# Kernel tuning notes

Measured on AMD Instinct MI355X. Metric: run time of the kernel, lower is better.

Reference implementation:

```python
import jax, jax.numpy as jnp
import numpy as np

B, T, S = 4, 2048, 512
HID, ND, NH = 2048, 1024, 16
HD = HID // NH  # 128
GATING_INIT = -4.0


def setup_inputs() -> dict:
    key = jax.random.key(0)
    ks = jax.random.split(key, 12)
    sc_h = 1.0 / np.sqrt(HID)
    sc_n = 1.0 / np.sqrt(ND)
    mask = jax.random.bernoulli(ks[2], 0.9, (B, S))
    mask = mask.at[:, 0].set(True)  # avoid fully-masked rows (NaN softmax)
    return {
        "hidden_states": jax.random.normal(ks[0], (B, T, HID), jnp.float32),
        "notes": jax.random.normal(ks[1], (B, S, ND), jnp.float32),
        "notes_mask": mask,
        "q_w": jax.random.normal(ks[3], (HID, HID), jnp.float32) * sc_h,
        "q_b": jax.random.normal(ks[4], (HID,), jnp.float32) * 0.01,
        "k_w": jax.random.normal(ks[5], (HID, ND), jnp.float32) * sc_n,
        "k_b": jax.random.normal(ks[6], (HID,), jnp.float32) * 0.01,
        "v_w": jax.random.normal(ks[7], (HID, ND), jnp.float32) * sc_n,
        "v_b": jax.random.normal(ks[8], (HID,), jnp.float32) * 0.01,
        "o_w": jax.random.normal(ks[9], (HID, HID), jnp.float32) * sc_h,
        "o_b": jax.random.normal(ks[10], (HID,), jnp.float32) * 0.01,
        "gate": jnp.full((1,), GATING_INIT, jnp.float32),
    }


def reference(hidden_states, notes, notes_mask, q_w, q_b, k_w, k_b, v_w, v_b, o_w, o_b, gate):
    # projections (torch Linear: x @ W^T + b)
    q = hidden_states @ q_w.T + q_b            # (B,T,HID)
    k = notes @ k_w.T + k_b                    # (B,S,HID)
    v = notes @ v_w.T + v_b                    # (B,S,HID)
    q = q.reshape(B, T, NH, HD).transpose(0, 2, 1, 3)  # (B,H,T,D)
    k = k.reshape(B, S, NH, HD).transpose(0, 2, 1, 3)  # (B,H,S,D)
    v = v.reshape(B, S, NH, HD).transpose(0, 2, 1, 3)
    scores = jnp.einsum("bhtd,bhsd->bhts", q, k) / jnp.sqrt(jnp.float32(HD))
    scores = jnp.where(notes_mask[:, None, None, :], scores, -jnp.inf)
    attn = jax.nn.softmax(scores, axis=-1)
    context = jnp.einsum("bhts,bhsd->bhtd", attn, v)   # (B,H,T,D)
    g = jax.nn.sigmoid(gate).reshape(1, 1, 1, 1)
    context = (g * context).transpose(0, 2, 1, 3).reshape(B, T, HID)
    delta = context @ o_w.T + o_b
    return delta
```

## Files before the change

kernel.cpp:

```cpp
#include <hip/hip_runtime.h>
#include <hip/hip_bf16.h>
#include <stdint.h>

#define B_ 4
#define T_ 2048
#define S_ 512
#define HID_ 2048
#define ND_ 1024
#define NH_ 16
#define HD_ 128

typedef unsigned short u16;
typedef __attribute__((ext_vector_type(8))) short bf16x8;
typedef __attribute__((ext_vector_type(4))) float f32x4;
typedef __attribute__((ext_vector_type(4))) float f4;
typedef __attribute__((ext_vector_type(4))) u16 us4;
typedef __attribute__((ext_vector_type(8))) u16 us8;

__device__ inline u16 f2bf(float f) {
  unsigned u = __builtin_bit_cast(unsigned, f);
  u += 0x7FFFu + ((u >> 16) & 1u);
  return (u16)(u >> 16);
}

__device__ inline f32x4 mfma16(bf16x8 a, bf16x8 b, f32x4 c) {
  return __builtin_amdgcn_mfma_f32_16x16x32_bf16(a, b, c, 0, 0, 0);
}

__device__ inline void gload_lds16(const u16* g, u16* l) {
  __builtin_amdgcn_global_load_lds(
      (const __attribute__((address_space(1))) unsigned int*)g,
      (__attribute__((address_space(3))) unsigned int*)l, 16, 0, 0);
}

__global__ __launch_bounds__(256) void convert_all(
    const float* __restrict__ h, const float* __restrict__ n,
    const float* __restrict__ qw, const float* __restrict__ kw,
    const float* __restrict__ vw, const float* __restrict__ ow,
    u16* __restrict__ dh, u16* __restrict__ dn, u16* __restrict__ dqw,
    u16* __restrict__ dkw, u16* __restrict__ dvw, u16* __restrict__ dow) {
  const int C0 = 4194304;
  const int C1 = C0 + 524288;
  const int C2 = C1 + 1048576;
  const int C3 = C2 + 524288;
  const int C4 = C3 + 524288;
  const int C5 = C4 + 1048576;
  for (int c = blockIdx.x * blockDim.x + threadIdx.x; c < C5;
       c += gridDim.x * blockDim.x) {
    const float* s; u16* d; int o;
    if (c < C0)      { s = h;  d = dh;  o = c; }
    else if (c < C1) { s = n;  d = dn;  o = c - C0; }
    else if (c < C2) { s = qw; d = dqw; o = c - C1; }
    else if (c < C3) { s = kw; d = dkw; o = c - C2; }
    else if (c < C4) { s = vw; d = dvw; o = c - C3; }
    else             { s = ow; d = dow; o = c - C4; }
    f4 v = ((const f4*)s)[o];
    us4 r = { f2bf(v[0]), f2bf(v[1]), f2bf(v[2]), f2bf(v[3]) };
    ((us4*)d)[o] = r;
  }
}

template <bool OUT_BF16>
__global__ __launch_bounds__(256) void gemm_bt(
    const u16* __restrict__ A, const u16* __restrict__ Bm,
    const float* __restrict__ bias, void* __restrict__ Cout,
    int M, int N, int K) {
  __shared__ u16 As[128 * 32];
  __shared__ u16 Bs[128 * 32];
  const int tid = threadIdx.x;
  const int lane = tid & 63;
  const int wave = tid >> 6;
  const int wr = (wave >> 1) * 64;
  const int wc = (wave & 1) * 64;
  const int c15 = lane & 15;
  const int g = lane >> 4;
  const int bx = blockIdx.x, by = blockIdx.y;

  const u16* gA = A + (size_t)(by * 128 + (tid >> 2)) * K + (tid & 3) * 8;
  const u16* gB = Bm + (size_t)(bx * 128 + (tid >> 2)) * K + (tid & 3) * 8;

  f32x4 acc[4][4];
#pragma unroll
  for (int i = 0; i < 4; ++i)
#pragma unroll
    for (int j = 0; j < 4; ++j) acc[i][j] = (f32x4){0.f, 0.f, 0.f, 0.f};

  for (int k0 = 0; k0 < K; k0 += 32) {
    gload_lds16(gA + k0, &As[wave * 512]);
    gload_lds16(gA + (size_t)64 * K + k0, &As[2048 + wave * 512]);
    gload_lds16(gB + k0, &Bs[wave * 512]);
    gload_lds16(gB + (size_t)64 * K + k0, &Bs[2048 + wave * 512]);
    __syncthreads();
    bf16x8 af[4], bfr[4];
#pragma unroll
    for (int mt = 0; mt < 4; ++mt)
      af[mt] = *(const bf16x8*)&As[(wr + mt * 16 + c15) * 32 + g * 8];
#pragma unroll
    for (int nt = 0; nt < 4; ++nt)
      bfr[nt] = *(const bf16x8*)&Bs[(wc + nt * 16 + c15) * 32 + g * 8];
#pragma unroll
    for (int mt = 0; mt < 4; ++mt)
#pragma unroll
      for (int nt = 0; nt < 4; ++nt)
        acc[mt][nt] = mfma16(af[mt], bfr[nt], acc[mt][nt]);
    __syncthreads();
  }

#pragma unroll
  for (int mt = 0; mt < 4; ++mt)
#pragma unroll
    for (int nt = 0; nt < 4; ++nt) {
      const int m = by * 128 + wr + mt * 16 + g * 4;
      const int n = bx * 128 + wc + nt * 16 + c15;
      const float bv = bias[n];
#pragma unroll
      for (int r = 0; r < 4; ++r) {
        const float v = acc[mt][nt][r] + bv;
        if (OUT_BF16)
          ((u16*)Cout)[(size_t)(m + r) * N + n] = f2bf(v);
        else
          ((float*)Cout)[(size_t)(m + r) * N + n] = v;
      }
    }
}

template <bool OUT_BF16>
__global__ __launch_bounds__(512, 2) void gemm256(
    const u16* __restrict__ A, const u16* __restrict__ Bm,
    const float* __restrict__ bias, void* __restrict__ Cout,
    int M, int N, int K) {
  extern __shared__ u16 lds[];
  const int tid = threadIdx.x;
  const int lane = tid & 63, wave = tid >> 6;
  const int wm = wave >> 2, wn = wave & 3;
  const int c15 = lane & 15, g = lane >> 4;
  const int bn = blockIdx.x, bm = blockIdx.y;
  const int NT = K >> 5;

  const int srow = tid >> 2;
  const int sx = (tid & 3) ^ ((srow >> 1) & 3);
  const u16* pa0 = A + (size_t)(bm * 256 + srow) * K + sx * 8;
  const u16* pa1 = A + (size_t)(bm * 256 + 128 + srow) * K + sx * 8;
  const u16* pb0 = Bm + (size_t)(bn * 256 + srow) * K + sx * 8;
  const u16* pb1 = Bm + (size_t)(bn * 256 + 128 + srow) * K + sx * 8;

  const int xr = (c15 >> 1) & 3;
  const int aoff = wm * 4096 + c15 * 32 + ((g ^ xr)) * 8;
  const int boff = 8192 + wn * 2048 + c15 * 32 + ((g ^ xr)) * 8;

  f32x4 acc[8][4];
#pragma unroll
  for (int i = 0; i < 8; ++i)
#pragma unroll
    for (int j = 0; j < 4; ++j) acc[i][j] = (f32x4){0.f, 0.f, 0.f, 0.f};

  {
    u16* sA = lds + wave * 512;
    u16* sB = lds + 8192 + wave * 512;
    gload_lds16(pa0, sA);          gload_lds16(pa1, sA + 4096);
    gload_lds16(pb0, sB);          gload_lds16(pb1, sB + 4096);
    pa0 += 32; pa1 += 32; pb0 += 32; pb1 += 32;
    gload_lds16(pa0, sA + 16384);  gload_lds16(pa1, sA + 20480);
    gload_lds16(pb0, sB + 16384);  gload_lds16(pb1, sB + 20480);
    pa0 += 32; pa1 += 32; pb0 += 32; pb1 += 32;
  }
  asm volatile("s_waitcnt vmcnt(4)" ::: "memory");
  __builtin_amdgcn_s_barrier();
  __builtin_amdgcn_sched_barrier(0);

  int curo = 0, stgo = 32768;
  for (int t = 0; t < NT; ++t) {
    const bool more = (t + 2 < NT);
    const u16* cb = lds + curo;
    bf16x8 a[4], b[4];
#pragma unroll
    for (int mf = 0; mf < 4; ++mf)
      a[mf] = *(const bf16x8*)(cb + aoff + mf * 512);
#pragma unroll
    for (int nf = 0; nf < 4; ++nf)
      b[nf] = *(const bf16x8*)(cb + boff + nf * 512);
    if (more) {
      gload_lds16(pa0, lds + stgo + wave * 512);
      gload_lds16(pa1, lds + stgo + 4096 + wave * 512);
    }
    __builtin_amdgcn_s_barrier();
    __builtin_amdgcn_sched_barrier(0);
    __builtin_amdgcn_s_setprio(1);
#pragma unroll
    for (int mf = 0; mf < 4; ++mf)
#pragma unroll
      for (int nf = 0; nf < 4; ++nf)
        acc[mf][nf] = mfma16(a[mf], b[nf], acc[mf][nf]);
    __builtin_amdgcn_s_setprio(0);
    __builtin_amdgcn_s_barrier();
    __builtin_amdgcn_sched_barrier(0);
    bf16x8 a2[4];
#pragma unroll
    for (int mf = 0; mf < 4; ++mf)
      a2[mf] = *(const bf16x8*)(cb + aoff + (4 + mf) * 512);
    if (more) {
      gload_lds16(pb0, lds + stgo + 8192 + wave * 512);
      gload_lds16(pb1, lds + stgo + 12288 + wave * 512);
      pa0 += 32; pa1 += 32; pb0 += 32; pb1 += 32;
    }
    __builtin_amdgcn_s_barrier();
    __builtin_amdgcn_sched_barrier(0);
    __builtin_amdgcn_s_setprio(1);
#pragma unroll
    for (int mf = 0; mf < 4; ++mf)
#pragma unroll
      for (int nf = 0; nf < 4; ++nf)
        acc[4 + mf][nf] = mfma16(a2[mf], b[nf], acc[4 + mf][nf]);
    __builtin_amdgcn_s_setprio(0);
    if (t < NT - 1) {
      if (more) asm volatile("s_waitcnt vmcnt(4)" ::: "memory");
      else      asm volatile("s_waitcnt vmcnt(0)" ::: "memory");
    }
    __builtin_amdgcn_s_barrier();
    __builtin_amdgcn_sched_barrier(0);
    curo = (curo == 32768) ? 0 : curo + 16384;
    stgo = (stgo == 32768) ? 0 : stgo + 16384;
  }

#pragma unroll
  for (int mf = 0; mf < 8; ++mf)
#pragma unroll
    for (int nf = 0; nf < 4; ++nf) {
      const int m = bm * 256 + wm * 128 + mf * 16 + g * 4;
      const int n = bn * 256 + wn * 64 + nf * 16 + c15;
      const float bv = bias[n];
#pragma unroll
      for (int r = 0; r < 4; ++r) {
        const float v = acc[mf][nf][r] + bv;
        if (OUT_BF16)
          ((u16*)Cout)[(size_t)(m + r) * N + n] = f2bf(v);
        else
          ((float*)Cout)[(size_t)(m + r) * N + n] = v;
      }
    }
}

__global__ __launch_bounds__(256) void transpose_v(const u16* __restrict__ v,
                                                   u16* __restrict__ vt) {
  __shared__ u16 tile[32][36];
  const int s0 = blockIdx.x * 32;
  const int bh = blockIdx.y;
  const int d0 = blockIdx.z * 32;
  const int b = bh >> 4, h = bh & 15;
  const int tid = threadIdx.x;
  const int sl = tid >> 3, dl = (tid & 7) * 4;
  us4 val = *(const us4*)(v + (size_t)(b * S_ + s0 + sl) * HID_ + h * HD_ + d0 + dl);
  *(us4*)&tile[sl][dl] = val;
  __syncthreads();
  const int dl2 = tid >> 3, sl2 = (tid & 7) * 4;
  us4 outv = { tile[sl2 + 0][dl2], tile[sl2 + 1][dl2],
               tile[sl2 + 2][dl2], tile[sl2 + 3][dl2] };
  *(us4*)(vt + ((size_t)bh * HD_ + d0 + dl2) * S_ + s0 + sl2) = outv;
}

__global__ __launch_bounds__(256) void attn_fwd(
    const u16* __restrict__ q, const u16* __restrict__ k,
    const u16* __restrict__ vt, const int* __restrict__ mask,
    const float* __restrict__ gate, u16* __restrict__ ctx) {
  __shared__ u16 smem[16384];
  __shared__ float addend[S_];
  __shared__ u16 p_lds[4][16][40];
  const int tid = threadIdx.x, lane = tid & 63, wave = tid >> 6;
  const int bh = blockIdx.y, b = bh >> 4, h = bh & 15;
  const int t0 = blockIdx.x * 64 + wave * 16;
  const int c15 = lane & 15, g = lane >> 4;

  const u16* kb  = k + (size_t)b * S_ * HID_ + h * HD_;
  const u16* vtb = vt + (size_t)bh * HD_ * S_;

  const u16* sp[4];
  int dj[4];
  u16* ldsbase;
  ptrdiff_t stride;
  if (wave < 2) {
    ldsbase = smem;
    stride = 32 * HID_;
#pragma unroll
    for (int i = 0; i < 4; ++i) {
      const int jj = wave * 4 + i;
      const int row = jj * 4 + (lane >> 4);
      const int cb = (lane & 15) * 16;
      const int cbp = cb ^ ((row & 7) << 4);
      sp[i] = kb + (size_t)row * HID_ + (cbp >> 1);
      dj[i] = jj * 512;
    }
  } else {
    ldsbase = smem + 8192;
    stride = 32;
#pragma unroll
    for (int i = 0; i < 4; ++i) {
      const int jj = (wave - 2) * 4 + i;
      const int row = jj * 8 + (lane >> 3);
      const int cb = (lane & 7) * 16;
      const int cbp = cb ^ ((row & 7) << 4);
      const int d = row * 2 + (cbp >> 6);
      sp[i] = vtb + (size_t)d * S_ + ((cbp & 63) >> 1);
      dj[i] = jj * 512;
    }
  }
#define STAGE(cur)                                            \
  do {                                                        \
    _Pragma("unroll") for (int i_ = 0; i_ < 4; ++i_) {        \
      gload_lds16(sp[i_], ldsbase + (cur) * 4096 + dj[i_]);   \
      sp[i_] += stride;                                       \
    }                                                         \
  } while (0)

  STAGE(0);

  for (int s = tid; s < S_; s += 256)
    addend[s] = mask[b * S_ + s] ? 0.f : -1e30f;

  const u16* qrow = q + (size_t)(b * T_ + t0 + c15) * HID_ + h * HD_;
  bf16x8 qf[4];
#pragma unroll
  for (int dc = 0; dc < 4; ++dc)
    qf[dc] = *(const bf16x8*)&qrow[dc * 32 + g * 8];

  const int ksw = (c15 & 7) << 4;
  int kcol[4];
#pragma unroll
  for (int dc = 0; dc < 4; ++dc)
    kcol[dc] = ((dc * 64 + g * 16) ^ ksw) >> 1;
  const int krow0 = c15 * 128, krow1 = (16 + c15) * 128;
  const int vsw = ((c15 >> 1) & 7) << 4;
  const int vcol = (((c15 & 1) * 64 + g * 16) ^ vsw) >> 1;
  const int vrow = (c15 >> 1) * 64;

  float m_run = -1e30f, l_run = 0.f;
  f32x4 ct[8];
#pragma unroll
  for (int i = 0; i < 8; ++i) ct[i] = (f32x4){0.f, 0.f, 0.f, 0.f};
  const float scale = 0.08838834764831845f;

  __syncthreads();

  for (int it = 0; it < 16; ++it) {
    const int cur = it & 1;
    if (it < 15) STAGE(cur ^ 1);
    const int s0 = it * 32;
    const u16* kt = smem + cur * 4096;
    const u16* vl = smem + 8192 + cur * 4096;

    f32x4 st0 = {0.f, 0.f, 0.f, 0.f}, st1 = {0.f, 0.f, 0.f, 0.f};
    __builtin_amdgcn_s_setprio(1);
#pragma unroll
    for (int dc = 0; dc < 4; ++dc) {
      bf16x8 ka0 = *(const bf16x8*)&kt[krow0 + kcol[dc]];
      bf16x8 ka1 = *(const bf16x8*)&kt[krow1 + kcol[dc]];
      st0 = mfma16(ka0, qf[dc], st0);
      st1 = mfma16(ka1, qf[dc], st1);
    }
    __builtin_amdgcn_s_setprio(0);

    float sc[8];
#pragma unroll
    for (int r = 0; r < 4; ++r) {
      sc[r]     = st0[r] * scale + addend[s0 + g * 4 + r];
      sc[4 + r] = st1[r] * scale + addend[s0 + 16 + g * 4 + r];
    }
    float tm = sc[0];
#pragma unroll
    for (int i = 1; i < 8; ++i) tm = fmaxf(tm, sc[i]);
    tm = fmaxf(tm, __shfl_xor(tm, 16));
    tm = fmaxf(tm, __shfl_xor(tm, 32));
    const float nm = fmaxf(m_run, tm);
    if (!__all(nm - m_run <= 8.f)) {
      const float corr = __expf(m_run - nm);
      l_run *= corr;
#pragma unroll
      for (int dt = 0; dt < 8; ++dt)
#pragma unroll
        for (int r = 0; r < 4; ++r) ct[dt][r] *= corr;
      m_run = nm;
    }
    float p[8], ps = 0.f;
#pragma unroll
    for (int i = 0; i < 8; ++i) { p[i] = __expf(sc[i] - m_run); ps += p[i]; }
    ps += __shfl_xor(ps, 16);
    ps += __shfl_xor(ps, 32);
    l_run += ps;

    us4 pk0 = { f2bf(p[0]), f2bf(p[1]), f2bf(p[2]), f2bf(p[3]) };
    us4 pk1 = { f2bf(p[4]), f2bf(p[5]), f2bf(p[6]), f2bf(p[7]) };
    *(us4*)&p_lds[wave][c15][g * 4] = pk0;
    *(us4*)&p_lds[wave][c15][16 + g * 4] = pk1;
    bf16x8 pf = *(const bf16x8*)&p_lds[wave][c15][g * 8];

    __builtin_amdgcn_s_setprio(1);
#pragma unroll
    for (int dt = 0; dt < 8; ++dt) {
      bf16x8 vf = *(const bf16x8*)&vl[(dt * 8) * 64 + vrow + vcol];
      ct[dt] = mfma16(vf, pf, ct[dt]);
    }
    __builtin_amdgcn_s_setprio(0);

    __syncthreads();
  }
#undef STAGE

  const float gsig = 1.f / (1.f + __expf(-gate[0]));
  const float inv = gsig / l_run;
  u16* c_lds = smem + wave * (16 * 136);
#pragma unroll
  for (int dt = 0; dt < 8; ++dt) {
    us4 o = { f2bf(ct[dt][0] * inv), f2bf(ct[dt][1] * inv),
              f2bf(ct[dt][2] * inv), f2bf(ct[dt][3] * inv) };
    *(us4*)&c_lds[c15 * 136 + dt * 16 + g * 4] = o;
  }
  u16* crow = ctx + (size_t)(b * T_ + t0) * HID_ + h * HD_;
#pragma unroll
  for (int rep = 0; rep < 4; ++rep) {
    const int tt = g + rep * 4;
    us8 valv = *(const us8*)&c_lds[tt * 136 + c15 * 8];
    *(us8*)&crow[(size_t)tt * HID_ + c15 * 8] = valv;
  }
}

extern "C" void kernel_launch(void* const* d_in, const int* in_sizes, int n_in,
                              void* d_out, int out_size, void* d_ws, size_t ws_size,
                              hipStream_t stream) {
  (void)in_sizes; (void)n_in; (void)out_size; (void)ws_size;
  const float* hs   = (const float*)d_in[0];
  const float* nts  = (const float*)d_in[1];
  const int*   mask = (const int*)d_in[2];
  const float* qw   = (const float*)d_in[3];
  const float* qb   = (const float*)d_in[4];
  const float* kw   = (const float*)d_in[5];
  const float* kbi  = (const float*)d_in[6];
  const float* vw   = (const float*)d_in[7];
  const float* vbi  = (const float*)d_in[8];
  const float* ow   = (const float*)d_in[9];
  const float* obi  = (const float*)d_in[10];
  const float* gate = (const float*)d_in[11];
  float* out = (float*)d_out;

  char* w = (char*)d_ws;
  u16* h_bf   = (u16*)(w + 0);
  u16* n_bf   = (u16*)(w + 33554432);
  u16* qw_bf  = (u16*)(w + 37748736);
  u16* kw_bf  = (u16*)(w + 46137344);
  u16* vw_bf  = (u16*)(w + 50331648);
  u16* ow_bf  = (u16*)(w + 54525952);
  u16* q_bf   = (u16*)(w + 62914560);
  u16* k_bf   = (u16*)(w + 96468992);
  u16* v_bf   = (u16*)(w + 104857600);
  u16* vt_bf  = (u16*)(w + 113246208);
  u16* ctx_bf = h_bf;

  hipFuncSetAttribute(reinterpret_cast<const void*>(&gemm256<true>),
                      hipFuncAttributeMaxDynamicSharedMemorySize, 98304);
  hipFuncSetAttribute(reinterpret_cast<const void*>(&gemm256<false>),
                      hipFuncAttributeMaxDynamicSharedMemorySize, 98304);

  convert_all<<<dim3(2048), dim3(256), 0, stream>>>(
      hs, nts, qw, kw, vw, ow, h_bf, n_bf, qw_bf, kw_bf, vw_bf, ow_bf);
  gemm_bt<true><<<dim3(16, 16), dim3(256), 0, stream>>>(
      n_bf, kw_bf, kbi, k_bf, 2048, 2048, 1024);
  gemm_bt<true><<<dim3(16, 16), dim3(256), 0, stream>>>(
      n_bf, vw_bf, vbi, v_bf, 2048, 2048, 1024);
  transpose_v<<<dim3(16, 64, 4), dim3(256), 0, stream>>>(v_bf, vt_bf);
  gemm256<true><<<dim3(8, 32), dim3(512), 98304, stream>>>(
      h_bf, qw_bf, qb, q_bf, 8192, 2048, 2048);
  attn_fwd<<<dim3(32, 64), dim3(256), 0, stream>>>(
      q_bf, k_bf, vt_bf, mask, gate, ctx_bf);
  gemm256<false><<<dim3(8, 32), dim3(512), 98304, stream>>>(
      ctx_bf, ow_bf, obi, out, 8192, 2048, 2048);
}
```

Measured before the change: 303.1 us.

## Switch attention to 32x32 MFMA with register P exchange; swizzle GEMM block order

The attention kernel now gives each wave 32 query rows and uses 32x32x16 bf16 MFMA for both QK^T and PV. The shared-memory round trip for P is replaced by packed bf16 conversion and a cross-half lane shuffle, and the V tile layout and swizzle are reworked to match. This halves the attention grid and cuts LDS traffic and reduction shuffles, at the cost of more registers per wave. The 256-tile GEMM also remaps block indices so consecutive blocks share B-matrix columns, aiming for better L2 reuse.

```diff
diff --git a/kernel.cpp b/kernel.cpp
--- a/kernel.cpp
+++ b/kernel.cpp
@@ -11,11 +11,14 @@
 #define HD_ 128
 
 typedef unsigned short u16;
+typedef unsigned int u32;
 typedef __attribute__((ext_vector_type(8))) short bf16x8;
 typedef __attribute__((ext_vector_type(4))) float f32x4;
+typedef __attribute__((ext_vector_type(16))) float f32x16;
 typedef __attribute__((ext_vector_type(4))) float f4;
 typedef __attribute__((ext_vector_type(4))) u16 us4;
 typedef __attribute__((ext_vector_type(8))) u16 us8;
+typedef __attribute__((ext_vector_type(4))) u32 u32x4;
 
 __device__ inline u16 f2bf(float f) {
   unsigned u = __builtin_bit_cast(unsigned, f);
@@ -23,8 +26,17 @@
   return (u16)(u >> 16);
 }
 
+__device__ inline u32 cvtpk(float lo, float hi) {
+  u32 r;
+  asm("v_cvt_pk_bf16_f32 %0, %1, %2" : "=v"(r) : "v"(lo), "v"(hi));
+  return r;
+}
+
 __device__ inline f32x4 mfma16(bf16x8 a, bf16x8 b, f32x4 c) {
   return __builtin_amdgcn_mfma_f32_16x16x32_bf16(a, b, c, 0, 0, 0);
+}
+__device__ inline f32x16 mfma32(bf16x8 a, bf16x8 b, f32x16 c) {
+  return __builtin_amdgcn_mfma_f32_32x32x16_bf16(a, b, c, 0, 0, 0);
 }
 
 __device__ inline void gload_lds16(const u16* g, u16* l) {
@@ -134,7 +146,9 @@
   const int lane = tid & 63, wave = tid >> 6;
   const int wm = wave >> 2, wn = wave & 3;
   const int c15 = lane & 15, g = lane >> 4;
-  const int bn = blockIdx.x, bm = blockIdx.y;
+  const int bid = blockIdx.y * gridDim.x + blockIdx.x;
+  const int sw = (bid & 7) * 32 + (bid >> 3);
+  const int bn = sw & 7, bm = sw >> 3;
   const int NT = K >> 5;
 
   const int srow = tid >> 2;
@@ -262,13 +276,12 @@
     const u16* __restrict__ q, const u16* __restrict__ k,
     const u16* __restrict__ vt, const int* __restrict__ mask,
     const float* __restrict__ gate, u16* __restrict__ ctx) {
-  __shared__ u16 smem[16384];
+  __shared__ u16 smem[17408];
   __shared__ float addend[S_];
-  __shared__ u16 p_lds[4][16][40];
   const int tid = threadIdx.x, lane = tid & 63, wave = tid >> 6;
   const int bh = blockIdx.y, b = bh >> 4, h = bh & 15;
-  const int t0 = blockIdx.x * 64 + wave * 16;
-  const int c15 = lane & 15, g = lane >> 4;
+  const int tw = blockIdx.x * 128 + wave * 32;
+  const int l31 = lane & 31, hi = lane >> 5;
 
   const u16* kb  = k + (size_t)b * S_ * HID_ + h * HD_;
   const u16* vtb = vt + (size_t)bh * HD_ * S_;
@@ -295,11 +308,10 @@
 #pragma unroll
     for (int i = 0; i < 4; ++i) {
       const int jj = (wave - 2) * 4 + i;
-      const int row = jj * 8 + (lane >> 3);
-      const int cb = (lane & 7) * 16;
-      const int cbp = cb ^ ((row & 7) << 4);
-      const int d = row * 2 + (cbp >> 6);
-      sp[i] = vtb + (size_t)d * S_ + ((cbp & 63) >> 1);
+      const int d = jj * 16 + (lane >> 2);
+      const int cb = (lane & 3) * 16;
+      const int cbp = cb ^ ((d & 3) << 4);
+      sp[i] = vtb + (size_t)d * S_ + (cbp >> 1);
       dj[i] = jj * 512;
     }
   }
@@ -316,26 +328,25 @@
   for (int s = tid; s < S_; s += 256)
     addend[s] = mask[b * S_ + s] ? 0.f : -1e30f;
 
-  const u16* qrow = q + (size_t)(b * T_ + t0 + c15) * HID_ + h * HD_;
-  bf16x8 qf[4];
-#pragma unroll
-  for (int dc = 0; dc < 4; ++dc)
-    qf[dc] = *(const bf16x8*)&qrow[dc * 32 + g * 8];
-
-  const int ksw = (c15 & 7) << 4;
-  int kcol[4];
-#pragma unroll
-  for (int dc = 0; dc < 4; ++dc)
-    kcol[dc] = ((dc * 64 + g * 16) ^ ksw) >> 1;
-  const int krow0 = c15 * 128, krow1 = (16 + c15) * 128;
-  const int vsw = ((c15 >> 1) & 7) << 4;
-  const int vcol = (((c15 & 1) * 64 + g * 16) ^ vsw) >> 1;
-  const int vrow = (c15 >> 1) * 64;
+  const u16* qrow = q + (size_t)(b * T_ + tw + l31) * HID_ + h * HD_;
+  bf16x8 qf[8];
+#pragma unroll
+  for (int dc = 0; dc < 8; ++dc)
+    qf[dc] = *(const bf16x8*)&qrow[dc * 16 + hi * 8];
+
+  int kofs[8];
+#pragma unroll
+  for (int dc = 0; dc < 8; ++dc)
+    kofs[dc] = l31 * 128 + (((dc * 32 + hi * 16) ^ ((l31 & 7) << 4)) >> 1);
+  const int vcol0 = ((hi * 16) ^ ((l31 & 3) << 4)) >> 1;
+  const int vcol1 = ((32 + hi * 16) ^ ((l31 & 3) << 4)) >> 1;
 
   float m_run = -1e30f, l_run = 0.f;
-  f32x4 ct[8];
-#pragma unroll
-  for (int i = 0; i < 8; ++i) ct[i] = (f32x4){0.f, 0.f, 0.f, 0.f};
+  f32x16 ct[4];
+#pragma unroll
+  for (int i = 0; i < 4; ++i)
+#pragma unroll
+    for (int r = 0; r < 16; ++r) ct[i][r] = 0.f;
   const float scale = 0.08838834764831845f;
 
   __syncthreads();
@@ -347,56 +358,67 @@
     const u16* kt = smem + cur * 4096;
     const u16* vl = smem + 8192 + cur * 4096;
 
-    f32x4 st0 = {0.f, 0.f, 0.f, 0.f}, st1 = {0.f, 0.f, 0.f, 0.f};
+    f32x16 st;
+#pragma unroll
+    for (int r = 0; r < 16; ++r) st[r] = 0.f;
     __builtin_amdgcn_s_setprio(1);
 #pragma unroll
-    for (int dc = 0; dc < 4; ++dc) {
-      bf16x8 ka0 = *(const bf16x8*)&kt[krow0 + kcol[dc]];
-      bf16x8 ka1 = *(const bf16x8*)&kt[krow1 + kcol[dc]];
-      st0 = mfma16(ka0, qf[dc], st0);
-      st1 = mfma16(ka1, qf[dc], st1);
+    for (int dc = 0; dc < 8; ++dc) {
+      bf16x8 kf = *(const bf16x8*)&kt[kofs[dc]];
+      st = mfma32(kf, qf[dc], st);
     }
     __builtin_amdgcn_s_setprio(0);
 
-    float sc[8];
-#pragma unroll
-    for (int r = 0; r < 4; ++r) {
-      sc[r]     = st0[r] * scale + addend[s0 + g * 4 + r];
-      sc[4 + r] = st1[r] * scale + addend[s0 + 16 + g * 4 + r];
+    float sc[16];
+#pragma unroll
+    for (int rq = 0; rq < 4; ++rq) {
+      f4 ad = *(const f4*)&addend[s0 + rq * 8 + hi * 4];
+#pragma unroll
+      for (int m = 0; m < 4; ++m)
+        sc[rq * 4 + m] = st[rq * 4 + m] * scale + ad[m];
     }
     float tm = sc[0];
 #pragma unroll
-    for (int i = 1; i < 8; ++i) tm = fmaxf(tm, sc[i]);
-    tm = fmaxf(tm, __shfl_xor(tm, 16));
+    for (int i = 1; i < 16; ++i) tm = fmaxf(tm, sc[i]);
     tm = fmaxf(tm, __shfl_xor(tm, 32));
     const float nm = fmaxf(m_run, tm);
     if (!__all(nm - m_run <= 8.f)) {
       const float corr = __expf(m_run - nm);
       l_run *= corr;
 #pragma unroll
-      for (int dt = 0; dt < 8; ++dt)
-#pragma unroll
-        for (int r = 0; r < 4; ++r) ct[dt][r] *= corr;
+      for (int db = 0; db < 4; ++db)
+#pragma unroll
+        for (int r = 0; r < 16; ++r) ct[db][r] *= corr;
       m_run = nm;
     }
-    float p[8], ps = 0.f;
-#pragma unroll
-    for (int i = 0; i < 8; ++i) { p[i] = __expf(sc[i] - m_run); ps += p[i]; }
-    ps += __shfl_xor(ps, 16);
+    float p[16], ps = 0.f;
+#pragma unroll
+    for (int i = 0; i < 16; ++i) { p[i] = __expf(sc[i] - m_run); ps += p[i]; }
     ps += __shfl_xor(ps, 32);
     l_run += ps;
 
-    us4 pk0 = { f2bf(p[0]), f2bf(p[1]), f2bf(p[2]), f2bf(p[3]) };
-    us4 pk1 = { f2bf(p[4]), f2bf(p[5]), f2bf(p[6]), f2bf(p[7]) };
-    *(us4*)&p_lds[wave][c15][g * 4] = pk0;
-    *(us4*)&p_lds[wave][c15][16 + g * 4] = pk1;
-    bf16x8 pf = *(const bf16x8*)&p_lds[wave][c15][g * 8];
+    u32 w[8], x[8];
+#pragma unroll
+    for (int q2 = 0; q2 < 4; ++q2) {
+      w[2 * q2]     = cvtpk(p[4 * q2],     p[4 * q2 + 1]);
+      w[2 * q2 + 1] = cvtpk(p[4 * q2 + 2], p[4 * q2 + 3]);
+    }
+#pragma unroll
+    for (int i = 0; i < 8; ++i) x[i] = __shfl_xor((int)w[i], 32);
+    const u32x4 f0 = hi ? (u32x4){x[2], x[3], w[2], w[3]}
+                        : (u32x4){w[0], w[1], x[0], x[1]};
+    const u32x4 f1 = hi ? (u32x4){x[6], x[7], w[6], w[7]}
+                        : (u32x4){w[4], w[5], x[4], x[5]};
+    const bf16x8 pf0 = __builtin_bit_cast(bf16x8, f0);
+    const bf16x8 pf1 = __builtin_bit_cast(bf16x8, f1);
 
     __builtin_amdgcn_s_setprio(1);
 #pragma unroll
-    for (int dt = 0; dt < 8; ++dt) {
-      bf16x8 vf = *(const bf16x8*)&vl[(dt * 8) * 64 + vrow + vcol];
-      ct[dt] = mfma16(vf, pf, ct[dt]);
+    for (int db = 0; db < 4; ++db) {
+      bf16x8 vf0 = *(const bf16x8*)&vl[db * 1024 + l31 * 32 + vcol0];
+      ct[db] = mfma32(vf0, pf0, ct[db]);
+      bf16x8 vf1 = *(const bf16x8*)&vl[db * 1024 + l31 * 32 + vcol1];
+      ct[db] = mfma32(vf1, pf1, ct[db]);
     }
     __builtin_amdgcn_s_setprio(0);
 
@@ -406,19 +428,21 @@
 
   const float gsig = 1.f / (1.f + __expf(-gate[0]));
   const float inv = gsig / l_run;
-  u16* c_lds = smem + wave * (16 * 136);
-#pragma unroll
-  for (int dt = 0; dt < 8; ++dt) {
-    us4 o = { f2bf(ct[dt][0] * inv), f2bf(ct[dt][1] * inv),
-              f2bf(ct[dt][2] * inv), f2bf(ct[dt][3] * inv) };
-    *(us4*)&c_lds[c15 * 136 + dt * 16 + g * 4] = o;
-  }
-  u16* crow = ctx + (size_t)(b * T_ + t0) * HID_ + h * HD_;
-#pragma unroll
-  for (int rep = 0; rep < 4; ++rep) {
-    const int tt = g + rep * 4;
-    us8 valv = *(const us8*)&c_lds[tt * 136 + c15 * 8];
-    *(us8*)&crow[(size_t)tt * HID_ + c15 * 8] = valv;
+  u16* c_lds = smem + wave * 4352;
+#pragma unroll
+  for (int db = 0; db < 4; ++db)
+#pragma unroll
+    for (int rq = 0; rq < 4; ++rq) {
+      us4 o = { f2bf(ct[db][rq * 4 + 0] * inv), f2bf(ct[db][rq * 4 + 1] * inv),
+                f2bf(ct[db][rq * 4 + 2] * inv), f2bf(ct[db][rq * 4 + 3] * inv) };
+      *(us4*)&c_lds[l31 * 136 + db * 32 + rq * 8 + hi * 4] = o;
+    }
+  u16* crow = ctx + (size_t)(b * T_ + tw) * HID_ + h * HD_;
+#pragma unroll
+  for (int rep = 0; rep < 8; ++rep) {
+    const int tt = (lane >> 4) + rep * 4;
+    us8 valv = *(const us8*)&c_lds[tt * 136 + (lane & 15) * 8];
+    *(us8*)&crow[(size_t)tt * HID_ + (lane & 15) * 8] = valv;
   }
 }
 
@@ -467,7 +491,7 @@
   transpose_v<<<dim3(16, 64, 4), dim3(256), 0, stream>>>(v_bf, vt_bf);
   gemm256<true><<<dim3(8, 32), dim3(512), 98304, stream>>>(
       h_bf, qw_bf, qb, q_bf, 8192, 2048, 2048);
-  attn_fwd<<<dim3(32, 64), dim3(256), 0, stream>>>(
+  attn_fwd<<<dim3(16, 64), dim3(256), 0, stream>>>(
       q_bf, k_bf, vt_bf, mask, gate, ctx_bf);
   gemm256<false><<<dim3(8, 32), dim3(512), 98304, stream>>>(
       ctx_bf, ow_bf, obi, out, 8192, 2048, 2048);
```

Measured after the change: 285.7 us. -5.7%, faster.
